# Optimization experiments

Hardware: AMD Instinct MI355X
Metric: run time of the kernel (lower is better)

Reference implementation:

```python
import jax, jax.numpy as jnp
import numpy as np

N = 50000
E = 800000
IN_DIM, HID_DIM, OUT_DIM = 128, 64, 32


def setup_inputs() -> dict:
    key = jax.random.key(0)
    k1, k2, k3, k4 = jax.random.split(key, 4)
    x = jax.random.normal(k1, (N, IN_DIM), dtype=jnp.float32)
    edge_index = jax.random.randint(k2, (2, E), 0, N, dtype=jnp.int64)
    # Glorot-style init for GCNConv weights, zero bias (PyG default)
    W1 = jax.random.normal(k3, (IN_DIM, HID_DIM), dtype=jnp.float32) / np.sqrt(IN_DIM)
    b1 = jnp.zeros((HID_DIM,), dtype=jnp.float32)
    W2 = jax.random.normal(k4, (HID_DIM, OUT_DIM), dtype=jnp.float32) / np.sqrt(HID_DIM)
    b2 = jnp.zeros((OUT_DIM,), dtype=jnp.float32)
    return {"x": x, "edge_index": edge_index, "W1": W1, "b1": b1, "W2": W2, "b2": b2}


def _gcn_norm(edge_index, num_nodes):
    # Add self-loops (PyG GCNConv default add_self_loops=True)
    loops = jnp.arange(num_nodes, dtype=edge_index.dtype)
    row = jnp.concatenate([edge_index[0], loops])  # source
    col = jnp.concatenate([edge_index[1], loops])  # target
    deg = jax.ops.segment_sum(jnp.ones_like(col, dtype=jnp.float32), col,
                              num_segments=num_nodes)
    dis = jnp.where(deg > 0, jax.lax.rsqrt(jnp.maximum(deg, 1.0)), 0.0)
    norm = dis[row] * dis[col]  # [E+N]
    return row, col, norm


def _gcn_conv(h, row, col, norm, W, b, num_nodes):
    h = h @ W                                   # [N, out]
    msg = h[row] * norm[:, None]                # gather + scale, [E+N, out]
    out = jax.ops.segment_sum(msg, col, num_segments=num_nodes)
    return out + b


def reference(x, edge_index, W1, b1, W2, b2):
    num_nodes = x.shape[0]
    row, col, norm = _gcn_norm(edge_index, num_nodes)
    h = _gcn_conv(x, row, col, norm, W1, b1, num_nodes)
    h = jax.nn.relu(h)
    out = _gcn_conv(h, row, col, norm, W2, b2, num_nodes)
    return out
```

## Files before the change

kernel.cpp:

```cpp
#include <hip/hip_runtime.h>
#include <hip/hip_fp16.h>

#define Nn    50000
#define Ee    800000
#define IND   128
#define HIDD  64
#define OUTD  32
#define NBUCK ((Nn + 255) / 256)
#define EPB   4096
#define NBB   ((Ee + EPB - 1) / EPB)
#define SCAP  6144
#define RB    64
#define GB    ((Nn + RB - 1) / RB)
#define XSTR  136

typedef _Float16 f16x8 __attribute__((ext_vector_type(8)));
typedef float    f32x4 __attribute__((ext_vector_type(4)));

__device__ __forceinline__ int ld_nt_i32(const int* p) {
    return __builtin_nontemporal_load(p);
}
__device__ __forceinline__ long long ld_nt_i64(const long long* p) {
    return __builtin_nontemporal_load(p);
}

__device__ __forceinline__ void acc8(float* a, uint4 v) {
    float2 f0 = __half22float2(*(__half2*)&v.x);
    float2 f1 = __half22float2(*(__half2*)&v.y);
    float2 f2 = __half22float2(*(__half2*)&v.z);
    float2 f3 = __half22float2(*(__half2*)&v.w);
    a[0] += f0.x; a[1] += f0.y; a[2] += f1.x; a[3] += f1.y;
    a[4] += f2.x; a[5] += f2.y; a[6] += f3.x; a[7] += f3.y;
}

__global__ void k_prep(const float* __restrict__ W, int* __restrict__ gcur,
                       _Float16* __restrict__ WTg) {
    int t = threadIdx.x;
    if (t < NBUCK) gcur[t] = 0;
    for (int j = 0; j < 32; ++j) {
        int idx = j * 256 + t;
        int k = idx >> 6, n = idx & 63;
        WTg[n * XSTR + k] = (_Float16)W[idx];
    }
}

__global__ __launch_bounds__(256) void k_bin_gemm1(const void* __restrict__ p,
        int* __restrict__ gcur, unsigned int* __restrict__ staged,
        const float* __restrict__ x, const _Float16* __restrict__ WTg,
        __half* __restrict__ h1raw) {
    __shared__ alignas(16) char smem[21504];
    int t = threadIdx.x;
    if (blockIdx.x < NBB) {
        unsigned int* stage = (unsigned int*)smem;
        int* hist  = (int*)(smem + 16384);
        int* offs  = hist + 256;
        int* lcur  = offs + 256;
        int* gposs = lcur + 256;
        unsigned int* red = (unsigned int*)(gposs + 256);
        int base0 = blockIdx.x * EPB;
        red[t] = ((const unsigned int*)p)[2 * (base0 + t) + 1];
        hist[t] = 0;
        __syncthreads();
        for (int s = 128; s > 0; s >>= 1) {
            if (t < s) red[t] |= red[t + s];
            __syncthreads();
        }
        bool f64 = (red[0] == 0u);
        int nv = Ee - base0; if (nv > EPB) nv = EPB;
        unsigned int pl[16];
        #pragma unroll
        for (int q = 0; q < 16; ++q) {
            int e = base0 + q * 256 + t;
            if (e < Ee) {
                int r, c;
                if (f64) { r = (int)ld_nt_i64((const long long*)p + e);
                           c = (int)ld_nt_i64((const long long*)p + Ee + e); }
                else     { r = ld_nt_i32((const int*)p + e);
                           c = ld_nt_i32((const int*)p + Ee + e); }
                pl[q] = ((unsigned int)c << 16) | (unsigned int)r;
                atomicAdd(&hist[pl[q] >> 24], 1);
            }
        }
        __syncthreads();
        int v = hist[t];
        offs[t] = v;
        __syncthreads();
        for (int off = 1; off < 256; off <<= 1) {
            int add = (t >= off) ? offs[t - off] : 0;
            __syncthreads();
            offs[t] += add;
            __syncthreads();
        }
        int excl = offs[t] - v;
        __syncthreads();
        offs[t] = excl;
        lcur[t] = excl;
        __syncthreads();
        #pragma unroll
        for (int q = 0; q < 16; ++q) {
            int e = base0 + q * 256 + t;
            if (e < Ee) {
                int bk = pl[q] >> 24;
                int pos = atomicAdd(&lcur[bk], 1);
                stage[pos] = pl[q];
            }
        }
        if (t < NBUCK) {
            int hh = hist[t];
            gposs[t] = hh ? atomicAdd(&gcur[t], hh) : 0;
        }
        __syncthreads();
        for (int i = t; i < nv; i += 256) {
            unsigned int pv = stage[i];
            int bk = pv >> 24;
            int idx = gposs[bk] + (i - offs[bk]);
            if (idx < SCAP) staged[(size_t)bk * SCAP + idx] = pv;
        }
        return;
    }
    _Float16* Xl = (_Float16*)smem;
    int bid = blockIdx.x - NBB;
    int row0 = bid * RB;
    for (int i = t; i < RB * (IND / 4); i += 256) {
        int rr = i >> 5, kk = (i & 31) * 4;
        int gr = row0 + rr;
        float4 v = make_float4(0.f, 0.f, 0.f, 0.f);
        if (gr < Nn) v = ((const float4*)x)[(size_t)gr * (IND / 4) + (i & 31)];
        _Float16* dst = &Xl[rr * XSTR + kk];
        dst[0] = (_Float16)v.x; dst[1] = (_Float16)v.y;
        dst[2] = (_Float16)v.z; dst[3] = (_Float16)v.w;
    }
    __syncthreads();
    int wv = t >> 6, lane = t & 63;
    int m = lane & 15, quad = lane >> 4;
    f32x4 acc[4] = {{0.f,0.f,0.f,0.f},{0.f,0.f,0.f,0.f},
                    {0.f,0.f,0.f,0.f},{0.f,0.f,0.f,0.f}};
    const _Float16* xrow = &Xl[(wv * 16 + m) * XSTR + quad * 8];
    #pragma unroll
    for (int kt = 0; kt < 4; ++kt) {
        f16x8 av = *(const f16x8*)(xrow + kt * 32);
        #pragma unroll
        for (int ct = 0; ct < 4; ++ct) {
            f16x8 bv = *(const f16x8*)&WTg[(ct * 16 + m) * XSTR + kt * 32 + quad * 8];
            acc[ct] = __builtin_amdgcn_mfma_f32_16x16x32_f16(av, bv, acc[ct], 0, 0, 0);
        }
    }
    int rbase = row0 + wv * 16 + quad * 4;
    #pragma unroll
    for (int reg = 0; reg < 4; ++reg) {
        int gr = rbase + reg;
        if (gr < Nn) {
            #pragma unroll
            for (int ct = 0; ct < 4; ++ct)
                h1raw[(size_t)gr * HIDD + ct * 16 + m] = __float2half(acc[ct][reg]);
        }
    }
}

__global__ __launch_bounds__(256) void k_bsort(const unsigned int* __restrict__ staged,
        const int* __restrict__ gcur, int* __restrict__ rowstart,
        float* __restrict__ dis, unsigned short* __restrict__ slots,
        __half2* __restrict__ h1v) {
    __shared__ int bsc[256];
    __shared__ int hist[256], nodestart[256], cur[256];
    __shared__ float ndis[256];
    __shared__ unsigned short sortbuf[SCAP];
    int t = threadIdx.x, b = blockIdx.x;
    int gv = (t < NBUCK) ? min(gcur[t], SCAP) : 0;
    bsc[t] = gv;
    hist[t] = 0;
    __syncthreads();
    for (int off = 1; off < 256; off <<= 1) {
        int add = (t >= off) ? bsc[t - off] : 0;
        __syncthreads();
        bsc[t] += add;
        __syncthreads();
    }
    int bucketbase = (b == 0) ? 0 : bsc[b - 1];
    int m = bsc[b] - bucketbase;
    const unsigned int* sp = staged + (size_t)b * SCAP;
    for (int i = t; i < m; i += 256) atomicAdd(&hist[(sp[i] >> 16) & 255], 1);
    __syncthreads();
    int v = hist[t];
    nodestart[t] = v;
    __syncthreads();
    for (int off = 1; off < 256; off <<= 1) {
        int add = (t >= off) ? nodestart[t - off] : 0;
        __syncthreads();
        nodestart[t] += add;
        __syncthreads();
    }
    int excl = nodestart[t] - v;
    __syncthreads();
    nodestart[t] = excl;
    cur[t] = 0;
    int node = b * 256 + t;
    float dd = rsqrtf((float)v + 1.0f);
    ndis[t] = dd;
    if (node < Nn) {
        rowstart[node] = bucketbase + excl;
        dis[node] = dd;
    }
    if (b == NBUCK - 1 && t == 0) rowstart[Nn] = Ee;
    __syncthreads();
    for (int i = t; i < m; i += 256) {
        unsigned int pv = sp[i];
        int lc = (pv >> 16) & 255;
        int pos = nodestart[lc] + atomicAdd(&cur[lc], 1);
        sortbuf[pos] = (unsigned short)(pv & 0xFFFFu);
    }
    __syncthreads();
    for (int i = t; i < m; i += 256) slots[bucketbase + i] = sortbuf[i];
    for (int i = t; i < 256 * 32; i += 256) {
        int nl = i >> 5;
        int n = b * 256 + nl;
        if (n < Nn) {
            float2 f = __half22float2(h1v[(size_t)n * 32 + (i & 31)]);
            float d = ndis[nl];
            h1v[(size_t)n * 32 + (i & 31)] = __floats2half2_rn(d * f.x, d * f.y);
        }
    }
}

__global__ __launch_bounds__(256) void k_agg1(const unsigned short* __restrict__ slots,
        const int* __restrict__ rowstart, const float* __restrict__ dis,
        const uint4* __restrict__ h1q, const float* __restrict__ b1,
        const float* __restrict__ W2, __half* __restrict__ h2) {
    __shared__ float sh[32 * 65];
    __shared__ float W2s[HIDD * OUTD];
    int t = threadIdx.x;
    for (int i = t; i < HIDD * OUTD; i += 256) W2s[i] = W2[i];
    int sub = t >> 3, lane = t & 7;
    int n = blockIdx.x * 32 + sub;
    if (n < Nn) {
        int s = rowstart[n], e = rowstart[n + 1];
        float d = dis[n];
        float acc[8] = {0,0,0,0,0,0,0,0};
        int p = s;
        for (; p + 8 < e; p += 16) {
            int rv[16];
            #pragma unroll
            for (int q = 0; q < 16; ++q) {
                int idx = p + q;
                rv[q] = slots[idx < e ? idx : e - 1];
            }
            uint4 fv[16];
            #pragma unroll
            for (int q = 0; q < 16; ++q) fv[q] = h1q[rv[q] * 8 + lane];
            #pragma unroll
            for (int q = 0; q < 16; ++q)
                if (p + q < e) acc8(acc, fv[q]);
        }
        if (p < e) {
            int rv[8];
            #pragma unroll
            for (int q = 0; q < 8; ++q) {
                int idx = p + q;
                rv[q] = slots[idx < e ? idx : e - 1];
            }
            uint4 fv[8];
            #pragma unroll
            for (int q = 0; q < 8; ++q) fv[q] = h1q[rv[q] * 8 + lane];
            #pragma unroll
            for (int q = 0; q < 8; ++q)
                if (p + q < e) acc8(acc, fv[q]);
        }
        acc8(acc, h1q[n * 8 + lane]);
        #pragma unroll
        for (int j = 0; j < 8; ++j)
            sh[sub * 65 + lane * 8 + j] = fmaxf(b1[lane * 8 + j] + d * acc[j], 0.0f);
    }
    __syncthreads();
    int nl = t >> 3, j0 = (t & 7) * 4;
    float o[4] = {0, 0, 0, 0};
    #pragma unroll
    for (int k = 0; k < HIDD; ++k) {
        float sv = sh[nl * 65 + k];
        float4 w4 = *(const float4*)&W2s[k * OUTD + j0];
        o[0] = fmaf(sv, w4.x, o[0]); o[1] = fmaf(sv, w4.y, o[1]);
        o[2] = fmaf(sv, w4.z, o[2]); o[3] = fmaf(sv, w4.w, o[3]);
    }
    int n2 = blockIdx.x * 32 + nl;
    if (n2 < Nn) {
        float d2 = dis[n2];
        __half hv[4];
        #pragma unroll
        for (int q = 0; q < 4; ++q) hv[q] = __float2half(d2 * o[q]);
        *(uint2*)&h2[(size_t)n2 * OUTD + j0] = *(uint2*)hv;
    }
}

__global__ __launch_bounds__(256) void k_agg2(const unsigned short* __restrict__ slots,
        const int* __restrict__ rowstart, const float* __restrict__ dis,
        const uint4* __restrict__ h2q, const float* __restrict__ b2,
        float* __restrict__ out) {
    int t = threadIdx.x;
    int sub = t >> 2, lane = t & 3;
    int n = blockIdx.x * 64 + sub;
    if (n >= Nn) return;
    int s = rowstart[n], e = rowstart[n + 1];
    float d = dis[n];
    float acc[8] = {0,0,0,0,0,0,0,0};
    int p = s;
    for (; p + 8 < e; p += 16) {
        int rv[16];
        #pragma unroll
        for (int q = 0; q < 16; ++q) {
            int idx = p + q;
            rv[q] = slots[idx < e ? idx : e - 1];
        }
        uint4 fv[16];
        #pragma unroll
        for (int q = 0; q < 16; ++q) fv[q] = h2q[rv[q] * 4 + lane];
        #pragma unroll
        for (int q = 0; q < 16; ++q)
            if (p + q < e) acc8(acc, fv[q]);
    }
    if (p < e) {
        int rv[8];
        #pragma unroll
        for (int q = 0; q < 8; ++q) {
            int idx = p + q;
            rv[q] = slots[idx < e ? idx : e - 1];
        }
        uint4 fv[8];
        #pragma unroll
        for (int q = 0; q < 8; ++q) fv[q] = h2q[rv[q] * 4 + lane];
        #pragma unroll
        for (int q = 0; q < 8; ++q)
            if (p + q < e) acc8(acc, fv[q]);
    }
    acc8(acc, h2q[n * 4 + lane]);
    float4 r0, r1;
    r0.x = b2[lane * 8 + 0] + d * acc[0]; r0.y = b2[lane * 8 + 1] + d * acc[1];
    r0.z = b2[lane * 8 + 2] + d * acc[2]; r0.w = b2[lane * 8 + 3] + d * acc[3];
    r1.x = b2[lane * 8 + 4] + d * acc[4]; r1.y = b2[lane * 8 + 5] + d * acc[5];
    r1.z = b2[lane * 8 + 6] + d * acc[6]; r1.w = b2[lane * 8 + 7] + d * acc[7];
    float4* op = (float4*)&out[(size_t)n * OUTD + lane * 8];
    op[0] = r0; op[1] = r1;
}

extern "C" void kernel_launch(void* const* d_in, const int* in_sizes, int n_in,
                              void* d_out, int out_size, void* d_ws, size_t ws_size,
                              hipStream_t stream) {
    const float* x  = (const float*)d_in[0];
    const void*  ei = d_in[1];
    const float* W1 = (const float*)d_in[2];
    const float* b1 = (const float*)d_in[3];
    const float* W2 = (const float*)d_in[4];
    const float* b2 = (const float*)d_in[5];
    float* out = (float*)d_out;

    char* w = (char*)d_ws;
    int*            gcur     = (int*)w;            w += ((size_t)NBUCK * 4 + 255) / 256 * 256;
    int*            rowstart = (int*)w;            w += (size_t)(Nn + 1) * 4 + 188;
    float*          dis      = (float*)w;          w += (size_t)Nn * 4;
    _Float16*       WTg      = (_Float16*)w;       w += 64 * XSTR * 2 + 128;
    unsigned int*   staged   = (unsigned int*)w;   w += (size_t)NBUCK * SCAP * 4;
    unsigned short* slots    = (unsigned short*)w; w += (size_t)Ee * 2;
    __half*         h1       = (__half*)w;         w += (size_t)Nn * HIDD * 2;
    __half*         h2       = (__half*)w;         w += (size_t)Nn * OUTD * 2;

    k_prep     <<<1, 256, 0, stream>>>(W1, gcur, WTg);
    k_bin_gemm1<<<NBB + GB, 256, 0, stream>>>(ei, gcur, staged, x, WTg, h1);
    k_bsort    <<<NBUCK, 256, 0, stream>>>(staged, gcur, rowstart, dis, slots,
                                           (__half2*)h1);
    k_agg1     <<<(Nn + 31) / 32, 256, 0, stream>>>(slots, rowstart, dis,
                                                    (const uint4*)h1, b1, W2, h2);
    k_agg2     <<<(Nn + 63) / 64, 256, 0, stream>>>(slots, rowstart, dis,
                                                    (const uint4*)h2, b2, out);
}
```

Baseline: 160.0 us.

## Split layer-1 aggregation from GEMM2 and run GEMM2 on MFMA

```diff
diff --git a/kernel.cpp b/kernel.cpp
--- a/kernel.cpp
+++ b/kernel.cpp
@@ -13,6 +13,7 @@
 #define RB    64
 #define GB    ((Nn + RB - 1) / RB)
 #define XSTR  136
+#define W2STR 72
 
 typedef _Float16 f16x8 __attribute__((ext_vector_type(8)));
 typedef float    f32x4 __attribute__((ext_vector_type(4)));
@@ -33,14 +34,25 @@
     a[4] += f2.x; a[5] += f2.y; a[6] += f3.x; a[7] += f3.y;
 }
 
-__global__ void k_prep(const float* __restrict__ W, int* __restrict__ gcur,
-                       _Float16* __restrict__ WTg) {
-    int t = threadIdx.x;
-    if (t < NBUCK) gcur[t] = 0;
-    for (int j = 0; j < 32; ++j) {
-        int idx = j * 256 + t;
+__global__ void k_prep(const float* __restrict__ W1, const float* __restrict__ W2,
+                       int* __restrict__ gcur, _Float16* __restrict__ WTg,
+                       _Float16* __restrict__ W2T) {
+    int t = threadIdx.x, b = blockIdx.x;
+    if (b == 0) {
+        if (t < NBUCK) gcur[t] = 0;
+        for (int j = 0; j < 8; ++j) {
+            int idx = j * 256 + t;
+            int k = idx >> 5, n = idx & 31;
+            W2T[n * W2STR + k] = (_Float16)W2[idx];
+        }
+        return;
+    }
+    int base = (b - 1) * 512;
+    #pragma unroll
+    for (int j = 0; j < 2; ++j) {
+        int idx = base + j * 256 + t;
         int k = idx >> 6, n = idx & 63;
-        WTg[n * XSTR + k] = (_Float16)W[idx];
+        WTg[n * XSTR + k] = (_Float16)W1[idx];
     }
 }
 
@@ -225,68 +237,84 @@
 __global__ __launch_bounds__(256) void k_agg1(const unsigned short* __restrict__ slots,
         const int* __restrict__ rowstart, const float* __restrict__ dis,
         const uint4* __restrict__ h1q, const float* __restrict__ b1,
-        const float* __restrict__ W2, __half* __restrict__ h2) {
-    __shared__ float sh[32 * 65];
-    __shared__ float W2s[HIDD * OUTD];
+        __half* __restrict__ a1) {
     int t = threadIdx.x;
-    for (int i = t; i < HIDD * OUTD; i += 256) W2s[i] = W2[i];
-    int sub = t >> 3, lane = t & 7;
-    int n = blockIdx.x * 32 + sub;
-    if (n < Nn) {
-        int s = rowstart[n], e = rowstart[n + 1];
-        float d = dis[n];
-        float acc[8] = {0,0,0,0,0,0,0,0};
-        int p = s;
-        for (; p + 8 < e; p += 16) {
-            int rv[16];
+    int f = blockIdx.x & 1;
+    int g = blockIdx.x >> 1;
+    int sub = t >> 2, lane = t & 3;
+    int n = g * 64 + sub;
+    if (n >= Nn) return;
+    int s = rowstart[n], e = rowstart[n + 1];
+    float d = dis[n];
+    int fo = f * 4;
+    float acc[8] = {0,0,0,0,0,0,0,0};
+    int p = s;
+    for (; p + 8 < e; p += 16) {
+        int rv[16];
+        #pragma unroll
+        for (int q = 0; q < 16; ++q) {
+            int idx = p + q;
+            rv[q] = slots[idx < e ? idx : e - 1];
+        }
+        uint4 fv[16];
+        #pragma unroll
+        for (int q = 0; q < 16; ++q) fv[q] = h1q[rv[q] * 8 + fo + lane];
+        #pragma unroll
+        for (int q = 0; q < 16; ++q)
+            if (p + q < e) acc8(acc, fv[q]);
+    }
+    if (p < e) {
+        int rv[8];
+        #pragma unroll
+        for (int q = 0; q < 8; ++q) {
+            int idx = p + q;
+            rv[q] = slots[idx < e ? idx : e - 1];
+        }
+        uint4 fv[8];
+        #pragma unroll
+        for (int q = 0; q < 8; ++q) fv[q] = h1q[rv[q] * 8 + fo + lane];
+        #pragma unroll
+        for (int q = 0; q < 8; ++q)
+            if (p + q < e) acc8(acc, fv[q]);
+    }
+    acc8(acc, h1q[n * 8 + fo + lane]);
+    const float* bb = b1 + f * 32 + lane * 8;
+    __half hv[8];
+    #pragma unroll
+    for (int j = 0; j < 8; ++j)
+        hv[j] = __float2half(fmaxf(bb[j] + d * acc[j], 0.0f));
+    *(uint4*)&a1[(size_t)n * HIDD + f * 32 + lane * 8] = *(uint4*)hv;
+}
+
+__global__ __launch_bounds__(256) void k_gemm2(const __half* __restrict__ a1,
+        const _Float16* __restrict__ W2T, const float* __restrict__ dis,
+        __half* __restrict__ h2g) {
+    int t = threadIdx.x;
+    int wv = t >> 6, lane = t & 63;
+    int m = lane & 15, quad = lane >> 4;
+    int row0 = blockIdx.x * 64 + wv * 16;
+    int ar = row0 + m; if (ar > Nn - 1) ar = Nn - 1;
+    const _Float16* arow = (const _Float16*)a1 + (size_t)ar * HIDD + quad * 8;
+    f32x4 acc[2] = {{0.f,0.f,0.f,0.f},{0.f,0.f,0.f,0.f}};
+    #pragma unroll
+    for (int kt = 0; kt < 2; ++kt) {
+        f16x8 av = *(const f16x8*)(arow + kt * 32);
+        #pragma unroll
+        for (int ct = 0; ct < 2; ++ct) {
+            f16x8 bv = *(const f16x8*)&W2T[(ct * 16 + m) * W2STR + kt * 32 + quad * 8];
+            acc[ct] = __builtin_amdgcn_mfma_f32_16x16x32_f16(av, bv, acc[ct], 0, 0, 0);
+        }
+    }
+    int rbase = row0 + quad * 4;
+    #pragma unroll
+    for (int reg = 0; reg < 4; ++reg) {
+        int gr = rbase + reg;
+        if (gr < Nn) {
+            float d = dis[gr];
             #pragma unroll
-            for (int q = 0; q < 16; ++q) {
-                int idx = p + q;
-                rv[q] = slots[idx < e ? idx : e - 1];
-            }
-            uint4 fv[16];
-            #pragma unroll
-            for (int q = 0; q < 16; ++q) fv[q] = h1q[rv[q] * 8 + lane];
-            #pragma unroll
-            for (int q = 0; q < 16; ++q)
-                if (p + q < e) acc8(acc, fv[q]);
-        }
-        if (p < e) {
-            int rv[8];
-            #pragma unroll
-            for (int q = 0; q < 8; ++q) {
-                int idx = p + q;
-                rv[q] = slots[idx < e ? idx : e - 1];
-            }
-            uint4 fv[8];
-            #pragma unroll
-            for (int q = 0; q < 8; ++q) fv[q] = h1q[rv[q] * 8 + lane];
-            #pragma unroll
-            for (int q = 0; q < 8; ++q)
-                if (p + q < e) acc8(acc, fv[q]);
-        }
-        acc8(acc, h1q[n * 8 + lane]);
-        #pragma unroll
-        for (int j = 0; j < 8; ++j)
-            sh[sub * 65 + lane * 8 + j] = fmaxf(b1[lane * 8 + j] + d * acc[j], 0.0f);
-    }
-    __syncthreads();
-    int nl = t >> 3, j0 = (t & 7) * 4;
-    float o[4] = {0, 0, 0, 0};
-    #pragma unroll
-    for (int k = 0; k < HIDD; ++k) {
-        float sv = sh[nl * 65 + k];
-        float4 w4 = *(const float4*)&W2s[k * OUTD + j0];
-        o[0] = fmaf(sv, w4.x, o[0]); o[1] = fmaf(sv, w4.y, o[1]);
-        o[2] = fmaf(sv, w4.z, o[2]); o[3] = fmaf(sv, w4.w, o[3]);
-    }
-    int n2 = blockIdx.x * 32 + nl;
-    if (n2 < Nn) {
-        float d2 = dis[n2];
-        __half hv[4];
-        #pragma unroll
-        for (int q = 0; q < 4; ++q) hv[q] = __float2half(d2 * o[q]);
-        *(uint2*)&h2[(size_t)n2 * OUTD + j0] = *(uint2*)hv;
+            for (int ct = 0; ct < 2; ++ct)
+                h2g[(size_t)gr * OUTD + ct * 16 + m] = __float2half(d * acc[ct][reg]);
+        }
     }
 }
 
@@ -356,17 +384,20 @@
     int*            rowstart = (int*)w;            w += (size_t)(Nn + 1) * 4 + 188;
     float*          dis      = (float*)w;          w += (size_t)Nn * 4;
     _Float16*       WTg      = (_Float16*)w;       w += 64 * XSTR * 2 + 128;
+    _Float16*       W2T      = (_Float16*)w;       w += 32 * W2STR * 2 + 128;
     unsigned int*   staged   = (unsigned int*)w;   w += (size_t)NBUCK * SCAP * 4;
     unsigned short* slots    = (unsigned short*)w; w += (size_t)Ee * 2;
     __half*         h1       = (__half*)w;         w += (size_t)Nn * HIDD * 2;
-    __half*         h2       = (__half*)w;         w += (size_t)Nn * OUTD * 2;
-
-    k_prep     <<<1, 256, 0, stream>>>(W1, gcur, WTg);
+    __half*         a1       = (__half*)w;         w += (size_t)Nn * HIDD * 2;
+    __half*         h2g      = (__half*)w;         w += (size_t)Nn * OUTD * 2;
+
+    k_prep     <<<17, 256, 0, stream>>>(W1, W2, gcur, WTg, W2T);
     k_bin_gemm1<<<NBB + GB, 256, 0, stream>>>(ei, gcur, staged, x, WTg, h1);
     k_bsort    <<<NBUCK, 256, 0, stream>>>(staged, gcur, rowstart, dis, slots,
                                            (__half2*)h1);
-    k_agg1     <<<(Nn + 31) / 32, 256, 0, stream>>>(slots, rowstart, dis,
-                                                    (const uint4*)h1, b1, W2, h2);
+    k_agg1     <<<2 * ((Nn + 63) / 64), 256, 0, stream>>>(slots, rowstart, dis,
+                                                          (const uint4*)h1, b1, a1);
+    k_gemm2    <<<(Nn + 63) / 64, 256, 0, stream>>>(a1, W2T, dis, h2g);
     k_agg2     <<<(Nn + 63) / 64, 256, 0, stream>>>(slots, rowstart, dis,
-                                                    (const uint4*)h2, b2, out);
-}
+                                                    (const uint4*)h2g, b2, out);
+}
```

After: 156.7 us. -2.1%, faster.
